# Kernel optimization log

Hardware: AMD Instinct MI355X
Metric: run time of the kernel (lower is better)

Reference implementation:

```python
import jax, jax.numpy as jnp
import numpy as np

NUM_CLASSES = 80
INF = 1e8
STRIDES = (8, 16, 32, 64, 128)
REG = ((0.0, 64.0), (64.0, 128.0), (128.0, 256.0), (256.0, 512.0), (512.0, INF))
GRAY_F = (0.9, 1.1)
FM = ((128, 128), (64, 64), (32, 32), (16, 16), (8, 8))  # 1024x1024 input


def _build_level_constants():
    pts, rr, gr, st = [], [], [], []
    for (h, w), s, (lo, up) in zip(FM, STRIDES, REG):
        xs = np.arange(w, dtype=np.float32) * s
        ys = np.arange(h, dtype=np.float32) * s
        ym, xm = np.meshgrid(ys, xs, indexing='ij')
        n = h * w
        pts.append(np.stack([xm.ravel(), ym.ravel()], axis=-1))
        rr.append(np.tile(np.array([lo, up], np.float32), (n, 1)))
        gr.append(np.tile(np.array([lo * GRAY_F[0], up * GRAY_F[1]], np.float32), (n, 1)))
        st.append(np.full((n,), s, np.float32))
    cat = lambda a: jnp.asarray(np.concatenate(a, axis=0))
    return cat(pts), cat(rr), cat(gr), cat(st)


def setup_inputs() -> dict:
    key = jax.random.key(0)
    k1, k2, k3, k4 = jax.random.split(key, 4)
    B, G = 8, 100
    x0 = jax.random.uniform(k1, (B, G, 1), minval=0.0, maxval=900.0)
    y0 = jax.random.uniform(k2, (B, G, 1), minval=0.0, maxval=900.0)
    wh = jax.random.uniform(k3, (B, G, 2), minval=8.0, maxval=512.0)
    gt_bboxes = jnp.concatenate([x0, y0, wh], axis=-1)  # xywh
    gt_labels = jax.random.randint(k4, (B, G), 0, NUM_CLASSES)
    points, reg_ranges, gray_ranges, strides = _build_level_constants()
    return dict(gt_bboxes=gt_bboxes, gt_labels=gt_labels, points=points,
                reg_ranges=reg_ranges, gray_ranges=gray_ranges, strides=strides)


def _single_image(gt_bboxes, gt_labels, points, reg_ranges, gray_ranges, strides):
    # gt_bboxes [G,4] (x,y,w,h); points [P,2]; returns [P, C+4]
    px = points[:, 0:1]                      # [P,1]
    py = points[:, 1:2]
    x0 = gt_bboxes[None, :, 0]               # [1,G]
    y0 = gt_bboxes[None, :, 1]
    w = gt_bboxes[None, :, 2]
    h = gt_bboxes[None, :, 3]
    cx = x0 + w / 2.0
    cy = y0 + h / 2.0
    half = strides[:, None] / 2.0            # [P,1]

    xs = jnp.abs(px - cx) / half
    xs = jnp.where(xs >= 1.0, xs, 1.0)       # == xs*(xs>=1) + (xs<1)
    ys = jnp.abs(py - cy) / half
    ys = jnp.where(ys >= 1.0, ys, 1.0)
    scores = jnp.sqrt(1.0 / xs) * jnp.sqrt(1.0 / ys)   # [P,G]

    dx1 = px - x0
    dy1 = py - y0
    dx2 = x0 + w - 1.0 - px
    dy2 = y0 + h - 1.0 - py
    delta = jnp.stack([dx1, dy1, dx2, dy2], axis=-1)   # [P,G,4]
    delta = delta / reg_ranges[:, 1][:, None, None]

    larger = jnp.maximum(w, h)               # [1,G]
    lo, up = reg_ranges[:, 0:1], reg_ranges[:, 1:2]      # [P,1]
    glo, gup = gray_ranges[:, 0:1], gray_ranges[:, 1:2]
    hit = jnp.min(delta, axis=-1) >= 0       # [P,G]
    green = (lo <= larger) & (larger <= up) & hit
    gray = (((glo <= larger) & (larger < lo)) | ((up < larger) & (larger <= gup))) & hit

    order = jnp.argsort(scores, axis=1)      # ascending, like torch.sort
    s_scores = jnp.take_along_axis(scores, order, axis=1)
    s_labels = jnp.take_along_axis(jnp.broadcast_to(gt_labels[None, :], scores.shape), order, axis=1)
    s_green = jnp.take_along_axis(green, order, axis=1)
    s_gray = jnp.take_along_axis(gray, order, axis=1)
    s_delta = jnp.take_along_axis(delta, order[..., None], axis=1)

    P = points.shape[0]
    rows = jnp.broadcast_to(jnp.arange(P)[:, None], s_labels.shape)
    cls = jnp.zeros((P, NUM_CLASSES), scores.dtype)
    cls = cls.at[rows, s_labels].max(jnp.where(s_green, s_scores, 0.0))
    gray_hit = jnp.zeros((P, NUM_CLASSES), scores.dtype)
    gray_hit = gray_hit.at[rows, s_labels].max(s_gray.astype(scores.dtype))
    cls = jnp.where(gray_hit > 0, -1.0, cls)  # gray writes happen after green

    filt = s_scores * (s_green & ~s_gray)
    sel = jnp.argmax(filt, axis=1)            # first max, like torch.max
    reg = jnp.take_along_axis(s_delta, sel[:, None, None], axis=1)[:, 0, :]  # [P,4]
    return jnp.concatenate([cls, reg], axis=-1)


def reference(gt_bboxes, gt_labels, points, reg_ranges, gray_ranges, strides):
    f = jax.vmap(lambda b, l: _single_image(b, l, points, reg_ranges, gray_ranges, strides))
    return f(gt_bboxes, gt_labels)
```

## Files before the change

kernel.cpp:

```cpp
#include <hip/hip_runtime.h>

#define ROWF 84

__global__ __launch_bounds__(64) void lfd_assign_kernel(
    const float* __restrict__ gt_bboxes,
    const int*   __restrict__ gt_labels,
    const float* __restrict__ points,
    const float* __restrict__ reg_ranges,
    const float* __restrict__ gray_ranges,
    const float* __restrict__ strides,
    float* __restrict__ out,
    int G, int P)
{
    extern __shared__ float lds[];
    float*    rows  = lds;
    float4*   boxA  = (float4*)(lds + 64 * ROWF);
    float2*   ctr   = (float2*)(boxA + G);
    unsigned* clist = (unsigned*)(ctr + ((G + 1) & ~1));

    const int tid = threadIdx.x;
    const int b   = blockIdx.y;
    const int p   = blockIdx.x * 64 + tid;

    const float px  = points[p * 2 + 0];
    const float py  = points[p * 2 + 1];
    const float lo  = reg_ranges[p * 2 + 0];
    const float up  = reg_ranges[p * 2 + 1];
    const float glo = gray_ranges[p * 2 + 0];
    const float gup = gray_ranges[p * 2 + 1];
    const float inv_half = 2.0f / strides[p];
    const float inv_up   = 1.0f / up;

    bool i0 = false, gray0 = false, i1 = false, gray1 = false;
    int  lab0 = 0, lab1 = 0;
    {
        int g = tid;
        if (g < G) {
            const float4 bb = *(const float4*)(gt_bboxes + (size_t)(b * G + g) * 4);
            boxA[g] = make_float4(bb.x, bb.y, bb.x + bb.z - 1.0f, bb.y + bb.w - 1.0f);
            ctr[g]  = make_float2(bb.x + 0.5f * bb.z, bb.y + 0.5f * bb.w);
            const float larger = fmaxf(bb.z, bb.w);
            lab0 = gt_labels[b * G + g];
            const bool green = (lo <= larger) && (larger <= up);
            gray0 = ((glo <= larger) && (larger < lo)) || ((up < larger) && (larger <= gup));
            i0 = green || gray0;
        }
        g = tid + 64;
        if (g < G) {
            const float4 bb = *(const float4*)(gt_bboxes + (size_t)(b * G + g) * 4);
            boxA[g] = make_float4(bb.x, bb.y, bb.x + bb.z - 1.0f, bb.y + bb.w - 1.0f);
            ctr[g]  = make_float2(bb.x + 0.5f * bb.z, bb.y + 0.5f * bb.w);
            const float larger = fmaxf(bb.z, bb.w);
            lab1 = gt_labels[b * G + g];
            const bool green = (lo <= larger) && (larger <= up);
            gray1 = ((glo <= larger) && (larger < lo)) || ((up < larger) && (larger <= gup));
            i1 = green || gray1;
        }
    }
    const unsigned long long m0 = __ballot(i0);
    const unsigned long long m1 = __ballot(i1);
    const int c0 = __popcll(m0);
    const unsigned long long below = (1ull << tid) - 1ull;
    if (i0) clist[__popcll(m0 & below)] =
        (unsigned)tid | ((unsigned)lab0 << 8) | (gray0 ? 0x80000000u : 0u);
    if (i1) clist[c0 + __popcll(m1 & below)] =
        (unsigned)(tid + 64) | ((unsigned)lab1 << 8) | (gray1 ? 0x80000000u : 0u);
    const int ncomp = c0 + __popcll(m1);

    float* myrow = rows + tid * ROWF;
#pragma unroll
    for (int k = 0; k < 21; ++k)
        *reinterpret_cast<float4*>(myrow + 4 * k) = make_float4(0.f, 0.f, 0.f, 0.f);

    __syncthreads();

    const float4* ctr2 = (const float4*)ctr;
    float min_score = 1e30f; int min_g = 0;
    int g = 0;
#pragma unroll 4
    for (; g + 1 < G; g += 2) {
        const float4 c = ctr2[g >> 1];
        const float s0 = rsqrtf(fmaxf(fabsf(px - c.x) * inv_half, 1.0f) *
                                fmaxf(fabsf(py - c.y) * inv_half, 1.0f));
        const float s1 = rsqrtf(fmaxf(fabsf(px - c.z) * inv_half, 1.0f) *
                                fmaxf(fabsf(py - c.w) * inv_half, 1.0f));
        if (s0 < min_score) { min_score = s0; min_g = g; }
        if (s1 < min_score) { min_score = s1; min_g = g + 1; }
    }
    if (g < G) {
        const float2 c = ctr[g];
        const float s0 = rsqrtf(fmaxf(fabsf(px - c.x) * inv_half, 1.0f) *
                                fmaxf(fabsf(py - c.y) * inv_half, 1.0f));
        if (s0 < min_score) { min_score = s0; min_g = g; }
    }

    float best_score = 0.0f; int best_g = 0;
    unsigned gm0 = 0u, gm1 = 0u, gm2 = 0u;
    for (int i = 0; i < ncomp; ++i) {
        const unsigned e = clist[i];
        const int gg = (int)(e & 0xFFu);
        const float4 A = boxA[gg];
        const float d1 = px - A.x, d2 = py - A.y, d3 = A.z - px, d4 = A.w - py;
        if (fminf(fminf(d1, d2), fminf(d3, d4)) >= 0.0f) {
            const int label = (int)((e >> 8) & 0x7Fu);
            if (e & 0x80000000u) {
                if (label < 32)      gm0 |= 1u << label;
                else if (label < 64) gm1 |= 1u << (label - 32);
                else                 gm2 |= 1u << (label - 64);
            } else {
                const float2 c = ctr[gg];
                const float s = rsqrtf(fmaxf(fabsf(px - c.x) * inv_half, 1.0f) *
                                       fmaxf(fabsf(py - c.y) * inv_half, 1.0f));
                if (s > myrow[label]) myrow[label] = s;
                if (s > best_score) { best_score = s; best_g = gg; }
            }
        }
    }

    while (gm0) { const int c = __ffs(gm0) - 1; myrow[c]      = -1.0f; gm0 &= gm0 - 1u; }
    while (gm1) { const int c = __ffs(gm1) - 1; myrow[32 + c] = -1.0f; gm1 &= gm1 - 1u; }
    while (gm2) { const int c = __ffs(gm2) - 1; myrow[64 + c] = -1.0f; gm2 &= gm2 - 1u; }

    const int sel = (best_score > 0.0f) ? best_g : min_g;
    const float4 A = boxA[sel];
    myrow[80] = (px - A.x) * inv_up;
    myrow[81] = (py - A.y) * inv_up;
    myrow[82] = (A.z - px) * inv_up;
    myrow[83] = (A.w - py) * inv_up;

    __syncthreads();

    float4* dst = reinterpret_cast<float4*>(out + (size_t)(b * P + blockIdx.x * 64) * ROWF);
    const float4* src = reinterpret_cast<const float4*>(rows);
#pragma unroll
    for (int k = 0; k < 21; ++k)
        dst[k * 64 + tid] = src[k * 64 + tid];
}

extern "C" void kernel_launch(void* const* d_in, const int* in_sizes, int n_in,
                              void* d_out, int out_size, void* d_ws, size_t ws_size,
                              hipStream_t stream) {
    const float* gt_bboxes   = (const float*)d_in[0];
    const int*   gt_labels   = (const int*)d_in[1];
    const float* points      = (const float*)d_in[2];
    const float* reg_ranges  = (const float*)d_in[3];
    const float* gray_ranges = (const float*)d_in[4];
    const float* strides     = (const float*)d_in[5];
    float* out = (float*)d_out;

    const int P = in_sizes[5];
    const int B = out_size / (P * ROWF);
    const int G = in_sizes[1] / B;

    dim3 grid(P / 64, B);
    dim3 block(64);
    const size_t shmem = (size_t)(64 * ROWF) * sizeof(float)
                       + (size_t)G * sizeof(float4)
                       + (size_t)((G + 1) & ~1) * sizeof(float2)
                       + (size_t)G * sizeof(unsigned);
    lfd_assign_kernel<<<grid, block, shmem, stream>>>(
        gt_bboxes, gt_labels, points, reg_ranges, gray_ranges, strides, out, G, P);
}
```

Measured before the change: 37.41 us.

## Write assignment rows directly to global memory instead of staging in LDS

Drops the per-block shared-memory row buffer (64x84 floats). The output tile is now zeroed with coalesced global float4 stores, per-class max scores are applied with global integer atomicMax on the float bits, and gray markers and regression targets are stored straight to global. This removes the LDS copy-out pass and two block barriers, and cuts LDS use enough to allow far more resident blocks per CU. The cost is global atomics and scattered global stores in place of LDS updates, plus explicit vmcnt waits to keep each thread's zero-fill, atomic and overwrite steps in order.

```diff
diff --git a/kernel.cpp b/kernel.cpp
--- a/kernel.cpp
+++ b/kernel.cpp
@@ -13,8 +13,7 @@
     int G, int P)
 {
     extern __shared__ float lds[];
-    float*    rows  = lds;
-    float4*   boxA  = (float4*)(lds + 64 * ROWF);
+    float4*   boxA  = (float4*)lds;
     float2*   ctr   = (float2*)(boxA + G);
     unsigned* clist = (unsigned*)(ctr + ((G + 1) & ~1));
 
@@ -67,12 +66,11 @@
         (unsigned)(tid + 64) | ((unsigned)lab1 << 8) | (gray1 ? 0x80000000u : 0u);
     const int ncomp = c0 + __popcll(m1);
 
-    float* myrow = rows + tid * ROWF;
+    float4* dst4 = (float4*)(out + (size_t)(b * P + blockIdx.x * 64) * ROWF);
+    const float4 z4 = make_float4(0.f, 0.f, 0.f, 0.f);
 #pragma unroll
     for (int k = 0; k < 21; ++k)
-        *reinterpret_cast<float4*>(myrow + 4 * k) = make_float4(0.f, 0.f, 0.f, 0.f);
-
-    __syncthreads();
+        dst4[k * 64 + tid] = z4;
 
     const float4* ctr2 = (const float4*)ctr;
     float min_score = 1e30f; int min_g = 0;
@@ -94,6 +92,9 @@
         if (s0 < min_score) { min_score = s0; min_g = g; }
     }
 
+    asm volatile("s_waitcnt vmcnt(0)" ::: "memory");
+
+    float* myout = out + (size_t)(b * P + p) * ROWF;
     float best_score = 0.0f; int best_g = 0;
     unsigned gm0 = 0u, gm1 = 0u, gm2 = 0u;
     for (int i = 0; i < ncomp; ++i) {
@@ -111,30 +112,22 @@
                 const float2 c = ctr[gg];
                 const float s = rsqrtf(fmaxf(fabsf(px - c.x) * inv_half, 1.0f) *
                                        fmaxf(fabsf(py - c.y) * inv_half, 1.0f));
-                if (s > myrow[label]) myrow[label] = s;
+                atomicMax((int*)(myout + label), __float_as_int(s));
                 if (s > best_score) { best_score = s; best_g = gg; }
             }
         }
     }
 
-    while (gm0) { const int c = __ffs(gm0) - 1; myrow[c]      = -1.0f; gm0 &= gm0 - 1u; }
-    while (gm1) { const int c = __ffs(gm1) - 1; myrow[32 + c] = -1.0f; gm1 &= gm1 - 1u; }
-    while (gm2) { const int c = __ffs(gm2) - 1; myrow[64 + c] = -1.0f; gm2 &= gm2 - 1u; }
+    asm volatile("s_waitcnt vmcnt(0)" ::: "memory");
+
+    while (gm0) { const int c = __ffs(gm0) - 1; myout[c]      = -1.0f; gm0 &= gm0 - 1u; }
+    while (gm1) { const int c = __ffs(gm1) - 1; myout[32 + c] = -1.0f; gm1 &= gm1 - 1u; }
+    while (gm2) { const int c = __ffs(gm2) - 1; myout[64 + c] = -1.0f; gm2 &= gm2 - 1u; }
 
     const int sel = (best_score > 0.0f) ? best_g : min_g;
     const float4 A = boxA[sel];
-    myrow[80] = (px - A.x) * inv_up;
-    myrow[81] = (py - A.y) * inv_up;
-    myrow[82] = (A.z - px) * inv_up;
-    myrow[83] = (A.w - py) * inv_up;
-
-    __syncthreads();
-
-    float4* dst = reinterpret_cast<float4*>(out + (size_t)(b * P + blockIdx.x * 64) * ROWF);
-    const float4* src = reinterpret_cast<const float4*>(rows);
-#pragma unroll
-    for (int k = 0; k < 21; ++k)
-        dst[k * 64 + tid] = src[k * 64 + tid];
+    *(float4*)(myout + 80) = make_float4((px - A.x) * inv_up, (py - A.y) * inv_up,
+                                         (A.z - px) * inv_up, (A.w - py) * inv_up);
 }
 
 extern "C" void kernel_launch(void* const* d_in, const int* in_sizes, int n_in,
@@ -154,8 +147,7 @@
 
     dim3 grid(P / 64, B);
     dim3 block(64);
-    const size_t shmem = (size_t)(64 * ROWF) * sizeof(float)
-                       + (size_t)G * sizeof(float4)
+    const size_t shmem = (size_t)G * sizeof(float4)
                        + (size_t)((G + 1) & ~1) * sizeof(float2)
                        + (size_t)G * sizeof(unsigned);
     lfd_assign_kernel<<<grid, block, shmem, stream>>>(
```

New measurement: 33.90 us. 1.1x faster.
